# Performance work log

Measured on AMD Instinct MI355X. Metric: run time of the kernel, lower is better.

Reference implementation:

```python
import jax, jax.numpy as jnp
import numpy as np
from jax import lax

# MuSc core (post-ViT): multiscale avg-pooled patch features -> mutual pairwise
# distance scoring (leave-one-out over batch) -> top-min-k mean -> pixel map.
L_LAYERS = 4      # len(feature_layers)
B = 8             # batch (mutual-scoring reference pool)
PH = PW = 24      # 336 / patch 14
P = PH * PW       # 576 patches
D = 1024          # ViT-L embed dim
H = W = 336       # input image size
R_LIST = (1, 3, 5)
TOPMIN_MIN = 0.0
TOPMIN_MAX = 0.3


def setup_inputs() -> dict:
    key = jax.random.key(0)
    features = jax.random.normal(key, (L_LAYERS, B, P, D), dtype=jnp.float32)
    return {"features": features}


def _avg_pool_r(x, r):
    # x: [L, B, P, D]; AvgPool2d(r, stride=1, pad=r//2, count_include_pad=True)
    if r == 1:
        return x
    Ln, Bn, Pn, Dn = x.shape
    g = x.reshape(Ln, Bn, PH, PW, Dn)
    pad = r // 2
    s = lax.reduce_window(g, 0.0, lax.add,
                          (1, 1, r, r, 1), (1, 1, 1, 1, 1),
                          ((0, 0), (0, 0), (pad, pad), (pad, pad), (0, 0)))
    return (s / (r * r)).reshape(Ln, Bn, Pn, Dn)


def _msm_scores(feat):
    # feat: [L, B, P, D] L2-normalized. Mutual scoring (leave-one-out over B).
    sq = jnp.sum(feat * feat, axis=-1)                       # [L,B,P]
    dots = jnp.einsum('lbpd,lcqd->lbpcq', feat, feat)        # [L,B,P,B,P]
    d2 = sq[:, :, :, None, None] + sq[:, None, None, :, :] - 2.0 * dots
    d = jnp.sqrt(jnp.maximum(d2, 0.0))
    dmin = jnp.min(d, axis=-1)                               # [L,B,P,C] min over ref patches
    self_mask = jnp.eye(B, dtype=bool)[:, None, :]           # [B,1,C] exclude self image
    dmin = jnp.where(self_mask[None], jnp.inf, dmin)
    ds = jnp.sort(dmin, axis=-1)                             # ascending; self (inf) last
    ref = B - 1
    k_min = int(TOPMIN_MIN * ref)
    k_max = max(int(TOPMIN_MAX * ref), k_min + 1)
    return jnp.mean(ds[..., k_min:k_max], axis=-1)           # [L,B,P]


def _bilinear_ac(x, out_h, out_w):
    # align_corners=True bilinear upsample, x: [B, ph, pw]
    Bn, ph, pw = x.shape
    ys = jnp.arange(out_h, dtype=jnp.float32) * ((ph - 1) / (out_h - 1))
    xs = jnp.arange(out_w, dtype=jnp.float32) * ((pw - 1) / (out_w - 1))
    y0 = jnp.floor(ys).astype(jnp.int32); y1 = jnp.minimum(y0 + 1, ph - 1)
    x0 = jnp.floor(xs).astype(jnp.int32); x1 = jnp.minimum(x0 + 1, pw - 1)
    wy = (ys - y0)[None, :, None]
    wx = (xs - x0)[None, None, :]
    f00 = x[:, y0[:, None], x0[None, :]]
    f01 = x[:, y0[:, None], x1[None, :]]
    f10 = x[:, y1[:, None], x0[None, :]]
    f11 = x[:, y1[:, None], x1[None, :]]
    return (f00 * (1 - wy) * (1 - wx) + f01 * (1 - wy) * wx
            + f10 * wy * (1 - wx) + f11 * wy * wx)


def _forward(features):
    scores_r = []
    for r in R_LIST:  # small fixed multiscale loop
        f = _avg_pool_r(features, r)
        f = f / jnp.linalg.norm(f, axis=-1, keepdims=True)
        s = _msm_scores(f)                    # [L,B,P]
        scores_r.append(jnp.mean(s, axis=0))  # [B,P] mean over layers
    scores = jnp.mean(jnp.stack(scores_r, 0), axis=0)  # [B,P] mean over r
    scores_image = jnp.max(scores, axis=1)              # [B]
    scores_pixel = _bilinear_ac(scores.reshape(-1, PH, PW), H, W)  # [B,H,W]
    return scores_image, scores_pixel


def reference(features):
    return _forward(features)
```

## Files before the change

### kernel.cpp

```cpp
#include <hip/hip_runtime.h>
#include <stdint.h>

#define L_LAYERS 4
#define BATCH 8
#define PHH 24
#define PWW 24
#define PP (PHH*PWW)
#define DD 1024
#define ROWS (BATCH*PP)
#define OH 336
#define OW 336
#define NTILES 72
#define TT 36
#define NPAIRS (TT*(TT+1)/2)
#define NCOMBO 12
#define TOTBLK (NPAIRS*NCOMBO)
#define PRESCALE 1024.0f
#define INV_PRESCALE2_X2 (1.f/524288.f)

typedef __attribute__((ext_vector_type(8))) int i32x8;
typedef __attribute__((ext_vector_type(4))) float f32x4;

__device__ __forceinline__ unsigned int f2bf(float f) {
  unsigned int u = __float_as_uint(f);
  return (u + 0x7FFFu + ((u >> 16) & 1u)) >> 16;
}

__device__ __forceinline__ float bflo(unsigned int w) {
  return __uint_as_float(w << 16);
}
__device__ __forceinline__ float bfhi(unsigned int w) {
  return __uint_as_float(w & 0xFFFF0000u);
}

__device__ __forceinline__ void load4bf(float* d, const unsigned short* p) {
  const uint2 u = *(const uint2*)p;
  d[0] = bflo(u.x); d[1] = bfhi(u.x);
  d[2] = bflo(u.y); d[3] = bfhi(u.y);
}

__device__ __forceinline__ void async16(const void* g, void* l) {
  __builtin_amdgcn_global_load_lds(
      (const __attribute__((address_space(1))) void*)(size_t)(uintptr_t)g,
      (__attribute__((address_space(3))) void*)(uint32_t)(uintptr_t)l,
      16, 0, 0);
}

__global__ __launch_bounds__(256) void pool_kernel(
    const float* __restrict__ feat,
    unsigned short* __restrict__ h3,
    unsigned short* __restrict__ h5) {
  const int dch = blockIdx.x;
  const int b = blockIdx.y;
  const int l = blockIdx.z >> 1;
  const int half = blockIdx.z & 1;
  const int py0 = half * 12, py1 = py0 + 11;
  const int t = threadIdx.x;
  const int pxg = t >> 5;
  const int d2 = t & 31;

  __shared__ float ring[5][24 * 64];
  __shared__ unsigned int v3p[24 * 32];
  __shared__ unsigned int v5p[24 * 32];

  const float* fb = feat + ((size_t)l * BATCH + b) * PP * DD + dch * 64 + d2 * 2;

  for (int yy = py0 - 2; yy <= py0 + 1; ++yy) {
    if (yy < 0) continue;
    #pragma unroll
    for (int i = 0; i < 3; ++i) {
      int px = i * 8 + pxg;
      *(float2*)&ring[yy % 5][px * 64 + d2 * 2] =
          *(const float2*)(fb + (size_t)(yy * PWW + px) * DD);
    }
  }
  for (int py = py0; py <= py1; ++py) {
    const int yl = py + 2;
    if (yl < PHH) {
      __syncthreads();
      #pragma unroll
      for (int i = 0; i < 3; ++i) {
        int px = i * 8 + pxg;
        *(float2*)&ring[yl % 5][px * 64 + d2 * 2] =
            *(const float2*)(fb + (size_t)(yl * PWW + px) * DD);
      }
    }
    __syncthreads();
    #pragma unroll
    for (int i = 0; i < 3; ++i) {
      int px = i * 8 + pxg;
      float s3x = 0.f, s3y = 0.f, s5x = 0.f, s5y = 0.f;
      #pragma unroll
      for (int dy = -2; dy <= 2; ++dy) {
        int yy = py + dy;
        if (yy < 0 || yy >= PHH) continue;
        float2 v = *(const float2*)&ring[yy % 5][px * 64 + d2 * 2];
        s5x += v.x; s5y += v.y;
        if (dy >= -1 && dy <= 1) { s3x += v.x; s3y += v.y; }
      }
      v3p[px * 32 + d2] = f2bf(s3x) | (f2bf(s3y) << 16);
      v5p[px * 32 + d2] = f2bf(s5x) | (f2bf(s5y) << 16);
    }
    __syncthreads();
    #pragma unroll
    for (int i = 0; i < 3; ++i) {
      int px = i * 8 + pxg;
      float h3x = 0.f, h3y = 0.f, h5x = 0.f, h5y = 0.f;
      #pragma unroll
      for (int dx = -2; dx <= 2; ++dx) {
        int xx = px + dx;
        if (xx < 0 || xx >= PWW) continue;
        unsigned int w5 = v5p[xx * 32 + d2];
        h5x += bflo(w5); h5y += bfhi(w5);
        if (dx >= -1 && dx <= 1) {
          unsigned int w3 = v3p[xx * 32 + d2];
          h3x += bflo(w3); h3y += bfhi(w3);
        }
      }
      const size_t idx =
          ((size_t)l * ROWS + b * PP + py * PWW + px) * DD + dch * 64 + d2 * 2;
      *(unsigned int*)&h3[idx] = f2bf(h3x) | (f2bf(h3y) << 16);
      *(unsigned int*)&h5[idx] = f2bf(h5x) | (f2bf(h5y) << 16);
    }
  }
}

__global__ __launch_bounds__(256) void quant_kernel(
    const float* __restrict__ feat,
    const unsigned short* __restrict__ h3,
    const unsigned short* __restrict__ h5,
    unsigned char* __restrict__ nf_all) {
  const int row = blockIdx.x;
  const int l = blockIdx.y;
  const int t = threadIdx.x;
  const int lane = t & 63, w = t >> 6;
  const int d0 = t * 4;
  const size_t lro = ((size_t)l * ROWS + row) * DD + d0;

  float s1[4], s3[4], s5[4];
  {
    const float4 f = *(const float4*)(feat + lro);
    s1[0] = f.x; s1[1] = f.y; s1[2] = f.z; s1[3] = f.w;
  }
  load4bf(s3, h3 + lro);
  load4bf(s5, h5 + lro);

  float q1 = 0.f, q3 = 0.f, q5 = 0.f;
  #pragma unroll
  for (int j = 0; j < 4; ++j) {
    q1 += s1[j]*s1[j]; q3 += s3[j]*s3[j]; q5 += s5[j]*s5[j];
  }
  #pragma unroll
  for (int off = 32; off > 0; off >>= 1) {
    q1 += __shfl_down(q1, off);
    q3 += __shfl_down(q3, off);
    q5 += __shfl_down(q5, off);
  }
  __shared__ float red[4][3];
  if (lane == 0) { red[w][0] = q1; red[w][1] = q3; red[w][2] = q5; }
  __syncthreads();
  const float rn1 = rsqrtf(red[0][0] + red[1][0] + red[2][0] + red[3][0]) * PRESCALE;
  const float rn3 = rsqrtf(red[0][1] + red[1][1] + red[2][1] + red[3][1]) * PRESCALE;
  const float rn5 = rsqrtf(red[0][2] + red[1][2] + red[2][2] + red[3][2]) * PRESCALE;

  const size_t ro = (size_t)row * DD + d0;
  unsigned int o;
  o = __builtin_amdgcn_cvt_pk_fp8_f32(s1[0]*rn1, s1[1]*rn1, 0, false);
  o = __builtin_amdgcn_cvt_pk_fp8_f32(s1[2]*rn1, s1[3]*rn1, o, true);
  *(unsigned int*)(nf_all + (size_t)(0*L_LAYERS + l) * ROWS * DD + ro) = o;
  o = __builtin_amdgcn_cvt_pk_fp8_f32(s3[0]*rn3, s3[1]*rn3, 0, false);
  o = __builtin_amdgcn_cvt_pk_fp8_f32(s3[2]*rn3, s3[3]*rn3, o, true);
  *(unsigned int*)(nf_all + (size_t)(1*L_LAYERS + l) * ROWS * DD + ro) = o;
  o = __builtin_amdgcn_cvt_pk_fp8_f32(s5[0]*rn5, s5[1]*rn5, 0, false);
  o = __builtin_amdgcn_cvt_pk_fp8_f32(s5[2]*rn5, s5[3]*rn5, o, true);
  *(unsigned int*)(nf_all + (size_t)(2*L_LAYERS + l) * ROWS * DD + ro) = o;
}

__global__ __launch_bounds__(256, 3) void gemm_max_kernel(
    const unsigned char* __restrict__ nf_all,
    float* __restrict__ part) {
  const int bid = blockIdx.x;
  const int slot = (bid & 7) * (TOTBLK / 8) + (bid >> 3);
  const int combo = slot / NPAIRS;
  int rem = slot % NPAIRS;
  int it = 0;
  while (rem >= TT - it) { rem -= TT - it; ++it; }
  const int jt = it + rem;
  const int row0 = it * 128;
  const int col0 = jt * 128;

  {
    const bool inA = (row0 / PP) == ((row0 + 127) / PP);
    const bool inB = (col0 / PP) == ((col0 + 127) / PP);
    if (inA && inB && (row0 / PP) == (col0 / PP)) return;
  }

  __shared__ unsigned char As[128 * 128];
  __shared__ unsigned char Bs[128 * 128];

  const int t = threadIdx.x;
  const int lane = t & 63;
  const int wave = t >> 6;
  const int wm = wave >> 1;
  const int wn = wave & 1;

  const unsigned char* nf = nf_all + (size_t)combo * ROWS * DD;
  float* partialL = part + (size_t)combo * ROWS * NTILES;

  const f32x4 zero = {0.f, 0.f, 0.f, 0.f};
  f32x4 acc[4][4];
  #pragma unroll
  for (int m = 0; m < 4; ++m)
    #pragma unroll
    for (int n = 0; n < 4; ++n) acc[m][n] = zero;

  const unsigned char* gA = nf + (size_t)row0 * DD;
  const unsigned char* gB = nf + (size_t)col0 * DD;

  const int r15 = lane & 15;
  const int loff = ((((lane >> 4) << 1) ^ (r15 & 6)) << 4);
  const unsigned char* Abase = As + (size_t)(wm * 64 + r15) * 128 + loff;
  const unsigned char* Bbase = Bs + (size_t)(wn * 64 + r15) * 128 + loff;

  for (int kt = 0; kt < DD / 128; ++kt) {
    const int k0 = kt * 128;
    #pragma unroll
    for (int i = 0; i < 4; ++i) {
      int c = i * 256 + t;
      int row = c >> 3, j = c & 7;
      int g = j ^ (row & 6);
      async16(gA + (size_t)row * DD + k0 + g * 16, &As[c * 16]);
    }
    #pragma unroll
    for (int i = 0; i < 4; ++i) {
      int c = i * 256 + t;
      int row = c >> 3, j = c & 7;
      int g = j ^ (row & 6);
      async16(gB + (size_t)row * DD + k0 + g * 16, &Bs[c * 16]);
    }
    __syncthreads();

    const i32x8 a0 = *(const i32x8*)(Abase +    0);
    const i32x8 a1 = *(const i32x8*)(Abase + 2048);
    const i32x8 a2 = *(const i32x8*)(Abase + 4096);
    const i32x8 a3 = *(const i32x8*)(Abase + 6144);
    #pragma unroll
    for (int n = 0; n < 4; ++n) {
      const i32x8 bn = *(const i32x8*)(Bbase + n * 2048);
      acc[0][n] = __builtin_amdgcn_mfma_scale_f32_16x16x128_f8f6f4(
          a0, bn, acc[0][n], 0, 0, 0, 0x7F7F7F7F, 0, 0x7F7F7F7F);
      acc[1][n] = __builtin_amdgcn_mfma_scale_f32_16x16x128_f8f6f4(
          a1, bn, acc[1][n], 0, 0, 0, 0x7F7F7F7F, 0, 0x7F7F7F7F);
      acc[2][n] = __builtin_amdgcn_mfma_scale_f32_16x16x128_f8f6f4(
          a2, bn, acc[2][n], 0, 0, 0, 0x7F7F7F7F, 0, 0x7F7F7F7F);
      acc[3][n] = __builtin_amdgcn_mfma_scale_f32_16x16x128_f8f6f4(
          a3, bn, acc[3][n], 0, 0, 0, 0x7F7F7F7F, 0, 0x7F7F7F7F);
    }
    __syncthreads();
  }

  #pragma unroll
  for (int m = 0; m < 4; ++m) {
    #pragma unroll
    for (int g = 0; g < 4; ++g) {
      float v = fmaxf(fmaxf(acc[m][0][g], acc[m][1][g]),
                      fmaxf(acc[m][2][g], acc[m][3][g]));
      v = fmaxf(v, __shfl_xor(v, 1));
      v = fmaxf(v, __shfl_xor(v, 2));
      v = fmaxf(v, __shfl_xor(v, 4));
      v = fmaxf(v, __shfl_xor(v, 8));
      if ((lane & 15) == 0) {
        int row = row0 + wm * 64 + m * 16 + (lane >> 4) * 4 + g;
        partialL[(size_t)row * NTILES + 2 * jt + wn] = v;
      }
    }
  }
  if (it != jt) {
    #pragma unroll
    for (int n = 0; n < 4; ++n) {
      float v = -1e30f;
      #pragma unroll
      for (int m = 0; m < 4; ++m)
        #pragma unroll
        for (int g = 0; g < 4; ++g) v = fmaxf(v, acc[m][n][g]);
      v = fmaxf(v, __shfl_xor(v, 16));
      v = fmaxf(v, __shfl_xor(v, 32));
      if (lane < 16) {
        int col = col0 + wn * 64 + n * 16 + lane;
        partialL[(size_t)col * NTILES + 2 * it + wm] = v;
      }
    }
  }
}

__global__ __launch_bounds__(256) void reduce_topk_kernel(
    const float* __restrict__ part,
    float* __restrict__ scores) {
  const int row = blockIdx.x * 256 + threadIdx.x;
  if (row >= ROWS) return;
  const int b = row / PP;
  float sum = 0.f;
  for (int k = 0; k < NCOMBO; ++k) {
    const float* pr = part + ((size_t)k * ROWS + row) * NTILES;
    float d1 = 1e30f, d2 = 1e30f;
    #pragma unroll
    for (int c = 0; c < BATCH; ++c) {
      if (c == b) continue;
      float md = pr[c * 9];
      #pragma unroll
      for (int q = 1; q < 9; ++q) md = fmaxf(md, pr[c * 9 + q]);
      float d = sqrtf(fmaxf(2.f - md * INV_PRESCALE2_X2, 0.f));
      if (d < d1) { d2 = d1; d1 = d; }
      else if (d < d2) { d2 = d; }
    }
    sum += 0.5f * (d1 + d2);
  }
  scores[row] = sum;
}

__global__ __launch_bounds__(256) void final_kernel(
    const float* __restrict__ scores, float* __restrict__ out) {
  const int bid = blockIdx.x;
  const int t = threadIdx.x;
  if (bid < (BATCH * OH * OW) / 256) {
    const int idx = bid * 256 + t;
    const int b = idx / (OH * OW);
    const int rem = idx % (OH * OW);
    const int y = rem / OW, x = rem % OW;
    const float sc = (float)(23.0 / 335.0);
    const float ys = y * sc, xs = x * sc;
    const int y0 = (int)floorf(ys), x0 = (int)floorf(xs);
    const float wy = ys - (float)y0, wx = xs - (float)x0;
    const int y1 = min(y0 + 1, PHH - 1), x1 = min(x0 + 1, PWW - 1);
    const float* sb = scores + b * PP;
    const float f00 = sb[y0 * PWW + x0], f01 = sb[y0 * PWW + x1];
    const float f10 = sb[y1 * PWW + x0], f11 = sb[y1 * PWW + x1];
    const float v = f00 * (1.f - wy) * (1.f - wx) + f01 * (1.f - wy) * wx +
                    f10 * wy * (1.f - wx) + f11 * wy * wx;
    out[8 + idx] = v * (1.f / 12.f);
  } else {
    const int b = bid - (BATCH * OH * OW) / 256;
    float m = -1e30f;
    for (int p = t; p < PP; p += 256) m = fmaxf(m, scores[b * PP + p]);
    #pragma unroll
    for (int off = 32; off > 0; off >>= 1) m = fmaxf(m, __shfl_down(m, off));
    __shared__ float red[4];
    if ((t & 63) == 0) red[t >> 6] = m;
    __syncthreads();
    if (t == 0)
      out[b] = fmaxf(fmaxf(red[0], red[1]), fmaxf(red[2], red[3])) * (1.f / 12.f);
  }
}

extern "C" void kernel_launch(void* const* d_in, const int* in_sizes, int n_in,
                              void* d_out, int out_size, void* d_ws, size_t ws_size,
                              hipStream_t stream) {
  const float* feat = (const float*)d_in[0];
  float* out = (float*)d_out;
  char* ws = (char*)d_ws;

  const size_t NF_BYTES   = (size_t)NCOMBO * ROWS * DD;
  const size_t PART_BYTES = (size_t)NCOMBO * ROWS * NTILES * 4;
  const size_t SCR_BYTES  = (size_t)ROWS * 4;
  const size_t H_BYTES    = (size_t)L_LAYERS * ROWS * DD * 2;
  unsigned char*  nf_all = (unsigned char*)ws;
  float*          part   = (float*)(ws + NF_BYTES);
  float*          scr    = (float*)(ws + NF_BYTES + PART_BYTES);
  unsigned short* h3     = (unsigned short*)(ws + NF_BYTES + PART_BYTES + SCR_BYTES);
  unsigned short* h5     = (unsigned short*)(ws + NF_BYTES + PART_BYTES + SCR_BYTES + H_BYTES);

  pool_kernel<<<dim3(16, BATCH, L_LAYERS * 2), 256, 0, stream>>>(feat, h3, h5);
  quant_kernel<<<dim3(ROWS, L_LAYERS), 256, 0, stream>>>(feat, h3, h5, nf_all);
  gemm_max_kernel<<<TOTBLK, 256, 0, stream>>>(nf_all, part);
  reduce_topk_kernel<<<(ROWS + 255) / 256, 256, 0, stream>>>(part, scr);
  final_kernel<<<(BATCH * OH * OW) / 256 + BATCH, 256, 0, stream>>>(scr, out);
}
```

Measured before the change: 351.7 us.

## Keep pooling row window in registers and split top-k reduce across combos

The pool kernel drops its shared-memory ring buffer for the vertical window and keeps five rows of float2 values in registers, shifting them each step. That removes one __syncthreads and the LDS round-trip per row. The top-k reduction now runs one block per combo (a grid 12 times larger) and writes per-combo scores, and a new small kernel then sums the 12 values per row. This raises parallelism in a reduction that used only 18 blocks, at the cost of one extra launch and a small extra buffer in the workspace.

```diff
diff --git a/kernel.cpp b/kernel.cpp
--- a/kernel.cpp
+++ b/kernel.cpp
@@ -59,45 +59,55 @@
   const int pxg = t >> 5;
   const int d2 = t & 31;
 
-  __shared__ float ring[5][24 * 64];
   __shared__ unsigned int v3p[24 * 32];
   __shared__ unsigned int v5p[24 * 32];
 
   const float* fb = feat + ((size_t)l * BATCH + b) * PP * DD + dch * 64 + d2 * 2;
 
-  for (int yy = py0 - 2; yy <= py0 + 1; ++yy) {
-    if (yy < 0) continue;
+  const float2 z2 = {0.f, 0.f};
+  float2 w0[3], w1[3], w2[3], w3[3], w4[3];
+  #pragma unroll
+  for (int i = 0; i < 3; ++i) { w0[i] = z2; w1[i] = z2; w2[i] = z2; w3[i] = z2; }
+
+  if (py0 - 2 >= 0) {
     #pragma unroll
     for (int i = 0; i < 3; ++i) {
       int px = i * 8 + pxg;
-      *(float2*)&ring[yy % 5][px * 64 + d2 * 2] =
-          *(const float2*)(fb + (size_t)(yy * PWW + px) * DD);
-    }
-  }
+      w0[i] = *(const float2*)(fb + (size_t)((py0 - 2) * PWW + px) * DD);
+    }
+  }
+  if (py0 - 1 >= 0) {
+    #pragma unroll
+    for (int i = 0; i < 3; ++i) {
+      int px = i * 8 + pxg;
+      w1[i] = *(const float2*)(fb + (size_t)((py0 - 1) * PWW + px) * DD);
+    }
+  }
+  #pragma unroll
+  for (int i = 0; i < 3; ++i) {
+    int px = i * 8 + pxg;
+    w2[i] = *(const float2*)(fb + (size_t)(py0 * PWW + px) * DD);
+    w3[i] = *(const float2*)(fb + (size_t)((py0 + 1) * PWW + px) * DD);
+  }
+
   for (int py = py0; py <= py1; ++py) {
-    const int yl = py + 2;
-    if (yl < PHH) {
-      __syncthreads();
+    if (py + 2 < PHH) {
       #pragma unroll
       for (int i = 0; i < 3; ++i) {
         int px = i * 8 + pxg;
-        *(float2*)&ring[yl % 5][px * 64 + d2 * 2] =
-            *(const float2*)(fb + (size_t)(yl * PWW + px) * DD);
+        w4[i] = *(const float2*)(fb + (size_t)((py + 2) * PWW + px) * DD);
       }
-    }
-    __syncthreads();
+    } else {
+      #pragma unroll
+      for (int i = 0; i < 3; ++i) w4[i] = z2;
+    }
     #pragma unroll
     for (int i = 0; i < 3; ++i) {
       int px = i * 8 + pxg;
-      float s3x = 0.f, s3y = 0.f, s5x = 0.f, s5y = 0.f;
-      #pragma unroll
-      for (int dy = -2; dy <= 2; ++dy) {
-        int yy = py + dy;
-        if (yy < 0 || yy >= PHH) continue;
-        float2 v = *(const float2*)&ring[yy % 5][px * 64 + d2 * 2];
-        s5x += v.x; s5y += v.y;
-        if (dy >= -1 && dy <= 1) { s3x += v.x; s3y += v.y; }
-      }
+      float s3x = w1[i].x + w2[i].x + w3[i].x;
+      float s3y = w1[i].y + w2[i].y + w3[i].y;
+      float s5x = w0[i].x + w1[i].x + w2[i].x + w3[i].x + w4[i].x;
+      float s5y = w0[i].y + w1[i].y + w2[i].y + w3[i].y + w4[i].y;
       v3p[px * 32 + d2] = f2bf(s3x) | (f2bf(s3y) << 16);
       v5p[px * 32 + d2] = f2bf(s5x) | (f2bf(s5y) << 16);
     }
@@ -113,14 +123,19 @@
         unsigned int w5 = v5p[xx * 32 + d2];
         h5x += bflo(w5); h5y += bfhi(w5);
         if (dx >= -1 && dx <= 1) {
-          unsigned int w3 = v3p[xx * 32 + d2];
-          h3x += bflo(w3); h3y += bfhi(w3);
+          unsigned int w3w = v3p[xx * 32 + d2];
+          h3x += bflo(w3w); h3y += bfhi(w3w);
         }
       }
       const size_t idx =
           ((size_t)l * ROWS + b * PP + py * PWW + px) * DD + dch * 64 + d2 * 2;
       *(unsigned int*)&h3[idx] = f2bf(h3x) | (f2bf(h3y) << 16);
       *(unsigned int*)&h5[idx] = f2bf(h5x) | (f2bf(h5y) << 16);
+    }
+    __syncthreads();
+    #pragma unroll
+    for (int i = 0; i < 3; ++i) {
+      w0[i] = w1[i]; w1[i] = w2[i]; w2[i] = w3[i]; w3[i] = w4[i];
     }
   }
 }
@@ -295,26 +310,34 @@
 
 __global__ __launch_bounds__(256) void reduce_topk_kernel(
     const float* __restrict__ part,
+    float* __restrict__ scores_k) {
+  const int row = blockIdx.x * 256 + threadIdx.x;
+  if (row >= ROWS) return;
+  const int k = blockIdx.y;
+  const int b = row / PP;
+  const float* pr = part + ((size_t)k * ROWS + row) * NTILES;
+  float d1 = 1e30f, d2 = 1e30f;
+  #pragma unroll
+  for (int c = 0; c < BATCH; ++c) {
+    if (c == b) continue;
+    float md = pr[c * 9];
+    #pragma unroll
+    for (int q = 1; q < 9; ++q) md = fmaxf(md, pr[c * 9 + q]);
+    float d = sqrtf(fmaxf(2.f - md * INV_PRESCALE2_X2, 0.f));
+    if (d < d1) { d2 = d1; d1 = d; }
+    else if (d < d2) { d2 = d; }
+  }
+  scores_k[(size_t)k * ROWS + row] = 0.5f * (d1 + d2);
+}
+
+__global__ __launch_bounds__(256) void sum_scores_kernel(
+    const float* __restrict__ scores_k,
     float* __restrict__ scores) {
   const int row = blockIdx.x * 256 + threadIdx.x;
   if (row >= ROWS) return;
-  const int b = row / PP;
   float sum = 0.f;
-  for (int k = 0; k < NCOMBO; ++k) {
-    const float* pr = part + ((size_t)k * ROWS + row) * NTILES;
-    float d1 = 1e30f, d2 = 1e30f;
-    #pragma unroll
-    for (int c = 0; c < BATCH; ++c) {
-      if (c == b) continue;
-      float md = pr[c * 9];
-      #pragma unroll
-      for (int q = 1; q < 9; ++q) md = fmaxf(md, pr[c * 9 + q]);
-      float d = sqrtf(fmaxf(2.f - md * INV_PRESCALE2_X2, 0.f));
-      if (d < d1) { d2 = d1; d1 = d; }
-      else if (d < d2) { d2 = d; }
-    }
-    sum += 0.5f * (d1 + d2);
-  }
+  #pragma unroll
+  for (int k = 0; k < NCOMBO; ++k) sum += scores_k[(size_t)k * ROWS + row];
   scores[row] = sum;
 }
 
@@ -362,16 +385,19 @@
   const size_t NF_BYTES   = (size_t)NCOMBO * ROWS * DD;
   const size_t PART_BYTES = (size_t)NCOMBO * ROWS * NTILES * 4;
   const size_t SCR_BYTES  = (size_t)ROWS * 4;
+  const size_t SCRK_BYTES = (size_t)NCOMBO * ROWS * 4;
   const size_t H_BYTES    = (size_t)L_LAYERS * ROWS * DD * 2;
   unsigned char*  nf_all = (unsigned char*)ws;
   float*          part   = (float*)(ws + NF_BYTES);
   float*          scr    = (float*)(ws + NF_BYTES + PART_BYTES);
-  unsigned short* h3     = (unsigned short*)(ws + NF_BYTES + PART_BYTES + SCR_BYTES);
-  unsigned short* h5     = (unsigned short*)(ws + NF_BYTES + PART_BYTES + SCR_BYTES + H_BYTES);
+  float*          scrk   = (float*)(ws + NF_BYTES + PART_BYTES + SCR_BYTES);
+  unsigned short* h3     = (unsigned short*)(ws + NF_BYTES + PART_BYTES + SCR_BYTES + SCRK_BYTES);
+  unsigned short* h5     = (unsigned short*)(ws + NF_BYTES + PART_BYTES + SCR_BYTES + SCRK_BYTES + H_BYTES);
 
   pool_kernel<<<dim3(16, BATCH, L_LAYERS * 2), 256, 0, stream>>>(feat, h3, h5);
   quant_kernel<<<dim3(ROWS, L_LAYERS), 256, 0, stream>>>(feat, h3, h5, nf_all);
   gemm_max_kernel<<<TOTBLK, 256, 0, stream>>>(nf_all, part);
-  reduce_topk_kernel<<<(ROWS + 255) / 256, 256, 0, stream>>>(part, scr);
+  reduce_topk_kernel<<<dim3(ROWS / 256, NCOMBO), 256, 0, stream>>>(part, scrk);
+  sum_scores_kernel<<<ROWS / 256, 256, 0, stream>>>(scrk, scr);
   final_kernel<<<(BATCH * OH * OW) / 256 + BATCH, 256, 0, stream>>>(scr, out);
 }
```

Measured after the change: 321.5 us. 1.09x faster.
